# Kernel tuning notes

Hardware: AMD Instinct MI355X
Metric: run time of the kernel (lower is better)

Reference implementation:

```python
import jax, jax.numpy as jnp
import numpy as np


def setup_inputs() -> dict:
    key = jax.random.key(0)
    k1, k2, k3 = jax.random.split(key, 3)
    N = 8192
    risk = jax.random.normal(k1, (N,), dtype=jnp.float32)
    os_ = jax.random.randint(k2, (N,), 0, 2, dtype=jnp.int32)
    os_time = jax.random.randint(k3, (N,), 0, 3650, dtype=jnp.int32)
    return {"risk": risk, "os": os_, "os_time": os_time}


def reference(risk, os, os_time):
    # Cox negative log partial likelihood (faithful to torch source).
    # R_matrix[i, j] = 1 if os_time[j] >= os_time[i]  (j is in risk set of i)
    theta = risk                      # [N]
    exp_theta = jnp.exp(theta)        # [N]
    R = os_time[None, :] >= os_time[:, None]            # [N, N] bool mask
    risk_set_sum = jnp.sum(jnp.where(R, exp_theta[None, :], jnp.float32(0.0)), axis=1)  # [N]
    ev = os.astype(jnp.float32)
    loss = -jnp.sum((theta - jnp.log(risk_set_sum)) * ev) / jnp.sum(os)
    return loss
```

## Files before the change

### kernel.cpp

```cpp
#include <hip/hip_runtime.h>
#include <math.h>


#define HSIZE 4096
#define T1 1024
#define SPT 2
#define T2 1024
#define NW1 (T1 / 64)
#define NW2 (T2 / 64)

__global__ __launch_bounds__(T1) void k_hist(
    const float* __restrict__ risk,
    const int*   __restrict__ os,
    const int*   __restrict__ os_time,
    float*       __restrict__ ws,
    int N, int HB)
{
    __shared__ float he[HSIZE];
    __shared__ float hc[HSIZE];
    __shared__ float wred[NW1];

    const int tid  = threadIdx.x;
    const int bid  = blockIdx.x;
    const int lane = tid & 63;
    const int wid  = tid >> 6;

    *(float4*)&he[tid * 4] = make_float4(0.f, 0.f, 0.f, 0.f);
    *(float4*)&hc[tid * 4] = make_float4(0.f, 0.f, 0.f, 0.f);

    const int i0 = (bid * T1 + tid) * SPT;
    float th[SPT]; int tt[SPT]; int ee[SPT]; bool va[SPT];
    if (i0 + SPT - 1 < N) {
        float2 r2 = *(const float2*)&risk[i0];
        int2   t2 = *(const int2*)&os_time[i0];
        int2   e2 = *(const int2*)&os[i0];
        th[0] = r2.x; th[1] = r2.y;
        tt[0] = t2.x; tt[1] = t2.y;
        ee[0] = e2.x; ee[1] = e2.y;
        va[0] = va[1] = true;
    } else {
        #pragma unroll
        for (int k = 0; k < SPT; ++k) {
            int i = i0 + k;
            va[k] = i < N;
            th[k] = va[k] ? risk[i] : 0.f;
            tt[k] = va[k] ? os_time[i] : 0;
            ee[k] = va[k] ? os[i] : 0;
        }
    }
    float ex[SPT];
    #pragma unroll
    for (int k = 0; k < SPT; ++k) ex[k] = __expf(th[k]);
    __syncthreads();

    #pragma unroll
    for (int k = 0; k < SPT; ++k) {
        if (va[k]) {
            atomicAdd(&he[tt[k]], ex[k]);
            if (ee[k]) atomicAdd(&hc[tt[k]], 1.0f);
        }
    }
    float num = 0.f;
    #pragma unroll
    for (int k = 0; k < SPT; ++k) if (va[k] && ee[k]) num += th[k];
    #pragma unroll
    for (int off = 32; off; off >>= 1) num += __shfl_down(num, off, 64);
    if (lane == 0) wred[wid] = num;
    __syncthreads();

    float* oe = ws + (size_t)bid * (2 * HSIZE);
    *(float4*)&oe[tid * 4]         = *(float4*)&he[tid * 4];
    *(float4*)&oe[HSIZE + tid * 4] = *(float4*)&hc[tid * 4];
    if (tid == 0) {
        float s = 0.f;
        #pragma unroll
        for (int w = 0; w < NW1; ++w) s += wred[w];
        ws[(size_t)HB * (2 * HSIZE) + bid] = s;
    }
}

template <int HBC>
__device__ __forceinline__ void k_final_body(
    const float* __restrict__ ws, float* __restrict__ out, int HB)
{
    __shared__ float wtot[NW2];
    __shared__ float wls[NW2];
    __shared__ float wcs[NW2];

    const int tid  = threadIdx.x;
    const int lane = tid & 63;
    const int wid  = tid >> 6;

    float4 e4 = make_float4(0.f, 0.f, 0.f, 0.f);
    float4 c4 = make_float4(0.f, 0.f, 0.f, 0.f);
    if constexpr (HBC > 0) {
        float4 ea[HBC], ca[HBC];
        #pragma unroll
        for (int b = 0; b < HBC; ++b) {
            const float* p = ws + (size_t)b * (2 * HSIZE);
            ea[b] = *(const float4*)&p[tid * 4];
            ca[b] = *(const float4*)&p[HSIZE + tid * 4];
        }
        #pragma unroll
        for (int b = 0; b < HBC; ++b) {
            e4.x += ea[b].x; e4.y += ea[b].y; e4.z += ea[b].z; e4.w += ea[b].w;
            c4.x += ca[b].x; c4.y += ca[b].y; c4.z += ca[b].z; c4.w += ca[b].w;
        }
    } else {
        for (int b = 0; b < HB; ++b) {
            const float* p = ws + (size_t)b * (2 * HSIZE);
            const float4 a = *(const float4*)&p[tid * 4];
            const float4 c = *(const float4*)&p[HSIZE + tid * 4];
            e4.x += a.x; e4.y += a.y; e4.z += a.z; e4.w += a.w;
            c4.x += c.x; c4.y += c.y; c4.z += c.z; c4.w += c.w;
        }
    }
    const int HBr = (HBC > 0) ? HBC : HB;

    float s3 = e4.w;
    float s2 = e4.z + s3;
    float s1 = e4.y + s2;
    float s0 = e4.x + s1;
    float incl = s0;
    #pragma unroll
    for (int off = 1; off < 64; off <<= 1) {
        float o = __shfl_down(incl, off, 64);
        if (lane + off < 64) incl += o;
    }
    float exclLane = __shfl_down(incl, 1, 64);
    if (lane == 63) exclLane = 0.f;
    if (lane == 0) wtot[wid] = incl;
    __syncthreads();
    float exclWave = 0.f;
    for (int w = wid + 1; w < NW2; ++w) exclWave += wtot[w];
    const float add = exclWave + exclLane;
    s0 += add; s1 += add; s2 += add; s3 += add;

    float lsum = 0.f;
    lsum += (c4.x > 0.f) ? c4.x * __logf(s0) : 0.f;
    lsum += (c4.y > 0.f) ? c4.y * __logf(s1) : 0.f;
    lsum += (c4.z > 0.f) ? c4.z * __logf(s2) : 0.f;
    lsum += (c4.w > 0.f) ? c4.w * __logf(s3) : 0.f;
    float csum = c4.x + c4.y + c4.z + c4.w;

    #pragma unroll
    for (int off = 32; off; off >>= 1) {
        lsum += __shfl_down(lsum, off, 64);
        csum += __shfl_down(csum, off, 64);
    }
    if (lane == 0) { wls[wid] = lsum; wcs[wid] = csum; }
    __syncthreads();
    if (tid == 0) {
        float L = 0.f, C = 0.f, S = 0.f;
        #pragma unroll
        for (int w = 0; w < NW2; ++w) { L += wls[w]; C += wcs[w]; }
        for (int b = 0; b < HBr; ++b) S += ws[(size_t)HBr * (2 * HSIZE) + b];
        out[0] = -(S - L) / C;
    }
}

template <int HBC>
__global__ __launch_bounds__(T2) void k_final(
    const float* __restrict__ ws, float* __restrict__ out)
{
    k_final_body<HBC>(ws, out, HBC);
}

__global__ __launch_bounds__(T2) void k_final_gen(
    const float* __restrict__ ws, float* __restrict__ out, int HB)
{
    k_final_body<0>(ws, out, HB);
}

extern "C" void kernel_launch(void* const* d_in, const int* in_sizes, int n_in,
                              void* d_out, int out_size, void* d_ws, size_t ws_size,
                              hipStream_t stream) {
    const float* risk    = (const float*)d_in[0];
    const int*   os      = (const int*)d_in[1];
    const int*   os_time = (const int*)d_in[2];
    float*       out     = (float*)d_out;
    float*       ws      = (float*)d_ws;
    const int N  = in_sizes[0];
    const int HB = (N + T1 * SPT - 1) / (T1 * SPT);

    k_hist<<<HB, T1, 0, stream>>>(risk, os, os_time, ws, N, HB);
    if (HB == 4)      k_final<4><<<1, T2, 0, stream>>>(ws, out);
    else if (HB == 8) k_final<8><<<1, T2, 0, stream>>>(ws, out);
    else              k_final_gen<<<1, T2, 0, stream>>>(ws, out, HB);
}
```

Measured before the change: 14.84 us.

## Fuse histogram and final scan into one cooperative kernel with grid sync

For N=8192 (4 blocks), the histogram and finalisation kernels are merged into one cooperative launch that uses a grid-wide sync. This removes the second kernel launch and its dependency gap. Block 0 keeps its own histogram in shared memory instead of writing it out and reading it back, and the per-block event-theta partials are summed in parallel rather than serially by thread 0. The cost is cooperative-launch and grid-barrier overhead, with a fallback to the two-kernel path if the cooperative launch fails.

After: 42.89 us. +189.1%, slower.

```diff
diff --git a/kernel.cpp b/kernel.cpp
--- a/kernel.cpp
+++ b/kernel.cpp
@@ -1,27 +1,22 @@
 #include <hip/hip_runtime.h>
+#include <hip/hip_cooperative_groups.h>
 #include <math.h>
+
+namespace cg = cooperative_groups;
 
 
 #define HSIZE 4096
 #define T1 1024
 #define SPT 2
-#define T2 1024
 #define NW1 (T1 / 64)
-#define NW2 (T2 / 64)
-
-__global__ __launch_bounds__(T1) void k_hist(
-    const float* __restrict__ risk,
-    const int*   __restrict__ os,
-    const int*   __restrict__ os_time,
-    float*       __restrict__ ws,
-    int N, int HB)
-{
-    __shared__ float he[HSIZE];
-    __shared__ float hc[HSIZE];
-    __shared__ float wred[NW1];
-
+
+
+__device__ __forceinline__ void phase1_hist(
+    const float* __restrict__ risk, const int* __restrict__ os,
+    const int* __restrict__ os_time, float* __restrict__ ws,
+    int N, int HBn, float* he, float* hc, float* wred, int bid)
+{
     const int tid  = threadIdx.x;
-    const int bid  = blockIdx.x;
     const int lane = tid & 63;
     const int wid  = tid >> 6;
 
@@ -68,54 +63,21 @@
     if (lane == 0) wred[wid] = num;
     __syncthreads();
 
-    float* oe = ws + (size_t)bid * (2 * HSIZE);
-    *(float4*)&oe[tid * 4]         = *(float4*)&he[tid * 4];
-    *(float4*)&oe[HSIZE + tid * 4] = *(float4*)&hc[tid * 4];
     if (tid == 0) {
         float s = 0.f;
         #pragma unroll
         for (int w = 0; w < NW1; ++w) s += wred[w];
-        ws[(size_t)HB * (2 * HSIZE) + bid] = s;
-    }
-}
-
-template <int HBC>
-__device__ __forceinline__ void k_final_body(
-    const float* __restrict__ ws, float* __restrict__ out, int HB)
-{
-    __shared__ float wtot[NW2];
-    __shared__ float wls[NW2];
-    __shared__ float wcs[NW2];
-
+        ws[(size_t)HBn * (2 * HSIZE) + bid] = s;
+    }
+}
+
+__device__ __forceinline__ void phase2_finish(
+    float4 e4, float4 c4, float Spart, float* __restrict__ out,
+    float* wtot, float* wls, float* wcs)
+{
     const int tid  = threadIdx.x;
     const int lane = tid & 63;
     const int wid  = tid >> 6;
-
-    float4 e4 = make_float4(0.f, 0.f, 0.f, 0.f);
-    float4 c4 = make_float4(0.f, 0.f, 0.f, 0.f);
-    if constexpr (HBC > 0) {
-        float4 ea[HBC], ca[HBC];
-        #pragma unroll
-        for (int b = 0; b < HBC; ++b) {
-            const float* p = ws + (size_t)b * (2 * HSIZE);
-            ea[b] = *(const float4*)&p[tid * 4];
-            ca[b] = *(const float4*)&p[HSIZE + tid * 4];
-        }
-        #pragma unroll
-        for (int b = 0; b < HBC; ++b) {
-            e4.x += ea[b].x; e4.y += ea[b].y; e4.z += ea[b].z; e4.w += ea[b].w;
-            c4.x += ca[b].x; c4.y += ca[b].y; c4.z += ca[b].z; c4.w += ca[b].w;
-        }
-    } else {
-        for (int b = 0; b < HB; ++b) {
-            const float* p = ws + (size_t)b * (2 * HSIZE);
-            const float4 a = *(const float4*)&p[tid * 4];
-            const float4 c = *(const float4*)&p[HSIZE + tid * 4];
-            e4.x += a.x; e4.y += a.y; e4.z += a.z; e4.w += a.w;
-            c4.x += c.x; c4.y += c.y; c4.z += c.z; c4.w += c.w;
-        }
-    }
-    const int HBr = (HBC > 0) ? HBC : HB;
 
     float s3 = e4.w;
     float s2 = e4.z + s3;
@@ -132,7 +94,7 @@
     if (lane == 0) wtot[wid] = incl;
     __syncthreads();
     float exclWave = 0.f;
-    for (int w = wid + 1; w < NW2; ++w) exclWave += wtot[w];
+    for (int w = wid + 1; w < NW1; ++w) exclWave += wtot[w];
     const float add = exclWave + exclLane;
     s0 += add; s1 += add; s2 += add; s3 += add;
 
@@ -143,33 +105,145 @@
     lsum += (c4.w > 0.f) ? c4.w * __logf(s3) : 0.f;
     float csum = c4.x + c4.y + c4.z + c4.w;
 
+    float ssum = Spart;
     #pragma unroll
     for (int off = 32; off; off >>= 1) {
         lsum += __shfl_down(lsum, off, 64);
         csum += __shfl_down(csum, off, 64);
-    }
-    if (lane == 0) { wls[wid] = lsum; wcs[wid] = csum; }
+        ssum += __shfl_down(ssum, off, 64);
+    }
+    if (lane == 0) { wls[wid] = lsum; wcs[wid] = csum; wtot[wid] = ssum; }
     __syncthreads();
     if (tid == 0) {
         float L = 0.f, C = 0.f, S = 0.f;
         #pragma unroll
-        for (int w = 0; w < NW2; ++w) { L += wls[w]; C += wcs[w]; }
-        for (int b = 0; b < HBr; ++b) S += ws[(size_t)HBr * (2 * HSIZE) + b];
+        for (int w = 0; w < NW1; ++w) { L += wls[w]; C += wcs[w]; S += wtot[w]; }
         out[0] = -(S - L) / C;
     }
 }
 
+
 template <int HBC>
-__global__ __launch_bounds__(T2) void k_final(
-    const float* __restrict__ ws, float* __restrict__ out)
-{
-    k_final_body<HBC>(ws, out, HBC);
-}
-
-__global__ __launch_bounds__(T2) void k_final_gen(
+__global__ __launch_bounds__(T1) void k_fused(
+    const float* __restrict__ risk,
+    const int*   __restrict__ os,
+    const int*   __restrict__ os_time,
+    float*       __restrict__ out,
+    float*       __restrict__ ws,
+    int N, int HBdyn)
+{
+    const int HBn = (HBC > 0) ? HBC : HBdyn;
+    __shared__ float he[HSIZE];
+    __shared__ float hc[HSIZE];
+    __shared__ float wred[NW1];
+    __shared__ float wls[NW1];
+    __shared__ float wcs[NW1];
+
+    const int tid = threadIdx.x;
+    const int bid = blockIdx.x;
+
+    phase1_hist(risk, os, os_time, ws, N, HBn, he, hc, wred, bid);
+
+    if (bid != 0) {
+        float* oe = ws + (size_t)bid * (2 * HSIZE);
+        *(float4*)&oe[tid * 4]         = *(float4*)&he[tid * 4];
+        *(float4*)&oe[HSIZE + tid * 4] = *(float4*)&hc[tid * 4];
+    }
+    __threadfence();
+    cg::this_grid().sync();
+
+    if (bid != 0) return;
+
+    __threadfence();
+
+    float Spart = (tid < HBn) ? ws[(size_t)HBn * (2 * HSIZE) + tid] : 0.f;
+
+    float4 e4 = *(float4*)&he[tid * 4];
+    float4 c4 = *(float4*)&hc[tid * 4];
+    if constexpr (HBC > 0) {
+        float4 ea[HBC > 1 ? HBC - 1 : 1], ca[HBC > 1 ? HBC - 1 : 1];
+        #pragma unroll
+        for (int b = 1; b < HBC; ++b) {
+            const float* p = ws + (size_t)b * (2 * HSIZE);
+            ea[b - 1] = *(const float4*)&p[tid * 4];
+            ca[b - 1] = *(const float4*)&p[HSIZE + tid * 4];
+        }
+        #pragma unroll
+        for (int b = 1; b < HBC; ++b) {
+            e4.x += ea[b-1].x; e4.y += ea[b-1].y; e4.z += ea[b-1].z; e4.w += ea[b-1].w;
+            c4.x += ca[b-1].x; c4.y += ca[b-1].y; c4.z += ca[b-1].z; c4.w += ca[b-1].w;
+        }
+    } else {
+        for (int b = 1; b < HBn; ++b) {
+            const float* p = ws + (size_t)b * (2 * HSIZE);
+            const float4 a = *(const float4*)&p[tid * 4];
+            const float4 c = *(const float4*)&p[HSIZE + tid * 4];
+            e4.x += a.x; e4.y += a.y; e4.z += a.z; e4.w += a.w;
+            c4.x += c.x; c4.y += c.y; c4.z += c.z; c4.w += c.w;
+        }
+    }
+    __syncthreads();
+    phase2_finish(e4, c4, Spart, out, wred, wls, wcs);
+}
+
+
+__global__ __launch_bounds__(T1) void k_hist(
+    const float* __restrict__ risk,
+    const int*   __restrict__ os,
+    const int*   __restrict__ os_time,
+    float*       __restrict__ ws,
+    int N, int HB)
+{
+    __shared__ float he[HSIZE];
+    __shared__ float hc[HSIZE];
+    __shared__ float wred[NW1];
+    const int tid = threadIdx.x;
+    const int bid = blockIdx.x;
+
+    phase1_hist(risk, os, os_time, ws, N, HB, he, hc, wred, bid);
+
+    float* oe = ws + (size_t)bid * (2 * HSIZE);
+    *(float4*)&oe[tid * 4]         = *(float4*)&he[tid * 4];
+    *(float4*)&oe[HSIZE + tid * 4] = *(float4*)&hc[tid * 4];
+}
+
+template <int HBC>
+__global__ __launch_bounds__(T1) void k_final(
     const float* __restrict__ ws, float* __restrict__ out, int HB)
 {
-    k_final_body<0>(ws, out, HB);
+    __shared__ float wtot[NW1];
+    __shared__ float wls[NW1];
+    __shared__ float wcs[NW1];
+    const int tid = threadIdx.x;
+    const int HBn = (HBC > 0) ? HBC : HB;
+
+    float Spart = (tid < HBn) ? ws[(size_t)HBn * (2 * HSIZE) + tid] : 0.f;
+
+    float4 e4 = make_float4(0.f, 0.f, 0.f, 0.f);
+    float4 c4 = make_float4(0.f, 0.f, 0.f, 0.f);
+    if constexpr (HBC > 0) {
+        float4 ea[HBC], ca[HBC];
+        #pragma unroll
+        for (int b = 0; b < HBC; ++b) {
+            const float* p = ws + (size_t)b * (2 * HSIZE);
+            ea[b] = *(const float4*)&p[tid * 4];
+            ca[b] = *(const float4*)&p[HSIZE + tid * 4];
+        }
+        #pragma unroll
+        for (int b = 0; b < HBC; ++b) {
+            e4.x += ea[b].x; e4.y += ea[b].y; e4.z += ea[b].z; e4.w += ea[b].w;
+            c4.x += ca[b].x; c4.y += ca[b].y; c4.z += ca[b].z; c4.w += ca[b].w;
+        }
+    } else {
+        for (int b = 0; b < HB; ++b) {
+            const float* p = ws + (size_t)b * (2 * HSIZE);
+            const float4 a = *(const float4*)&p[tid * 4];
+            const float4 c = *(const float4*)&p[HSIZE + tid * 4];
+            e4.x += a.x; e4.y += a.y; e4.z += a.z; e4.w += a.w;
+            c4.x += c.x; c4.y += c.y; c4.z += c.z; c4.w += c.w;
+        }
+    }
+    phase2_finish(e4, c4, Spart, out, wtot, wls, wcs);
 }
 
 extern "C" void kernel_launch(void* const* d_in, const int* in_sizes, int n_in,
@@ -180,11 +254,20 @@
     const int*   os_time = (const int*)d_in[2];
     float*       out     = (float*)d_out;
     float*       ws      = (float*)d_ws;
-    const int N  = in_sizes[0];
-    const int HB = (N + T1 * SPT - 1) / (T1 * SPT);
+    int N  = in_sizes[0];
+    int HB = (N + T1 * SPT - 1) / (T1 * SPT);
+
+    if (HB == 4) {
+        void* args[] = {(void*)&risk, (void*)&os, (void*)&os_time,
+                        (void*)&out, (void*)&ws, (void*)&N, (void*)&HB};
+        hipError_t e = hipLaunchCooperativeKernel(
+            reinterpret_cast<const void*>(&k_fused<4>),
+            dim3(HB), dim3(T1), args, 0, stream);
+        if (e == hipSuccess) return;
+    }
 
     k_hist<<<HB, T1, 0, stream>>>(risk, os, os_time, ws, N, HB);
-    if (HB == 4)      k_final<4><<<1, T2, 0, stream>>>(ws, out);
-    else if (HB == 8) k_final<8><<<1, T2, 0, stream>>>(ws, out);
-    else              k_final_gen<<<1, T2, 0, stream>>>(ws, out, HB);
-}
+    if (HB == 4)      k_final<4><<<1, T1, 0, stream>>>(ws, out, HB);
+    else if (HB == 8) k_final<8><<<1, T1, 0, stream>>>(ws, out, HB);
+    else              k_final<0><<<1, T1, 0, stream>>>(ws, out, HB);
+}
```
